# Performance work log

Hardware: AMD Instinct MI355X
Metric: run time of the kernel (lower is better)

The kernel has to match this reference:

```python
import jax, jax.numpy as jnp
jax.config.update("jax_enable_x64", True)
import numpy as np

BUCKETS = 2147483647  # max int32, as in fused_project call sites
HALF = BUCKETS >> 1
NGRAM_SIZE = 3
# sgnn partition boundaries: indices = [i*(i+1)/2 * P for i in range(n)] + [proj], P=112
IDX = [0, 112, 336, 672]


def _project(sig, mask, seeds):
    """One SgnnProjection partition.

    sig:   [B, M] int64 hash signatures in [0, BUCKETS) (padded ragged rows)
    mask:  [B, M] bool validity of each padded slot (ragged row structure)
    seeds: [H] int64 hash seeds
    returns [B, H] float32
    """
    # value = floormod(abs(sig * seed), buckets); center to [-half, half]
    v = jnp.abs(sig[None, :, :] * seeds[:, None, None]) % BUCKETS  # [H, B, M]
    v = v - jnp.where(v > HALF, BUCKETS, 0)
    vf = v.astype(jnp.float32) * mask[None].astype(jnp.float32)
    counts = jnp.maximum(mask.sum(-1), 1).astype(jnp.float32)  # [B], ragged row lengths
    mean = vf.sum(-1) / counts[None]  # [H, B]  (ragged reduce_mean)
    return (mean / HALF).T  # [B, H]


def setup_inputs() -> dict:
    key = jax.random.key(0)
    k1, k2, k3 = jax.random.split(key, 3)
    signatures = jax.random.randint(k1, (NGRAM_SIZE, 1024, 128), 0, BUCKETS, dtype=jnp.int64)
    mask = jax.random.bernoulli(k2, 0.7, (NGRAM_SIZE, 1024, 128))
    hash_seed = jax.random.randint(k3, (IDX[-1],), 1, BUCKETS, dtype=jnp.int64)
    return {"signatures": signatures, "mask": mask, "hash_seed": hash_seed}


def reference(signatures, mask, hash_seed):
    outs = [
        _project(signatures[i], mask[i], hash_seed[IDX[i]:IDX[i + 1]])
        for i in range(NGRAM_SIZE)
    ]
    return jnp.concatenate(outs, axis=-1).astype(jnp.float32)  # [B, 672]
```

## Files before the change

kernel.cpp:

```cpp
#include <hip/hip_runtime.h>


#define M31    2147483647u
#define HALF_B 1073741823u

__global__ __launch_bounds__(64) void sgnn_prep_kernel(
    const int* __restrict__ sig,
    const int* __restrict__ mask,
    unsigned* __restrict__ msig,
    float* __restrict__ invc,
    unsigned* __restrict__ cnt4)
{
    const int row = blockIdx.x;
    const int t   = threadIdx.x;
    const int g0  = row * 128 + t;
    const int g1  = g0 + 64;
    const int mk0 = mask[g0], mk1 = mask[g1];
    const unsigned v0 = (unsigned)sig[g0], v1 = (unsigned)sig[g1];

    const unsigned long long b0 = __ballot(mk0 != 0);
    const unsigned long long b1 = __ballot(mk1 != 0);
    const unsigned long long lt = (1ULL << t) - 1ULL;
    const int c0   = __popcll(b0);
    const int cnt  = c0 + __popcll(b1);
    const int pos0 = __popcll(b0 & lt);
    const int pos1 = c0 + __popcll(b1 & lt);

    const unsigned base = (unsigned)row * 128u;
    if (mk0) msig[base + pos0] = v0;
    if (mk1) msig[base + pos1] = v1;

    const int c4 = (cnt + 3) & ~3;
    if (cnt + t < c4) msig[base + cnt + t] = 0u;

    if (t == 0) {
        int c = (cnt < 1) ? 1 : cnt;
        invc[row] = 1.0f / ((float)c * 1073741823.0f);
        cnt4[row] = (unsigned)c4;
    }
}

__device__ __forceinline__ void acc_elem(unsigned sv ,
                                         unsigned seed ,
                                         unsigned long long& sum, unsigned& q) {
    const unsigned long long p2 =
        (unsigned long long)sv * (unsigned long long)seed + (unsigned long long)HALF_B;
    const unsigned lo = (unsigned)p2;
    const unsigned hi = (unsigned)(p2 >> 32);
    const unsigned s  = __builtin_amdgcn_alignbit(hi, lo, 31) + (lo & 0x7FFFFFFFu);
    q   += (s >= M31);
    sum += s;
}

__global__ __launch_bounds__(256, 4) void sgnn_main_kernel(
    const unsigned* __restrict__ msig,
    const float* __restrict__ invc,
    const unsigned* __restrict__ cnt4,
    const int* __restrict__ seeds,
    float* __restrict__ out,
    int nbatch)
{
    const unsigned tid  = threadIdx.x;
    const unsigned lane = tid & 63u;
    const unsigned W    = blockIdx.x * 4u + (tid >> 6);
    const unsigned b    = blockIdx.y;

    unsigned p, h0, hmax;
    if (W < 2u)      { p = 0; h0 = W * 64u;              hmax = 112u; }
    else if (W < 6u) { p = 1; h0 = 112u + (W - 2u) * 64u; hmax = 336u; }
    else             { p = 2; h0 = 336u + (W - 6u) * 64u; hmax = 672u; }

    const unsigned h     = h0 + lane;
    const bool     valid = (h < hmax);
    const unsigned h_c   = valid ? h : (hmax - 1u);

    const unsigned row_u = __builtin_amdgcn_readfirstlane(p * (unsigned)nbatch + b);
    const unsigned* __restrict__ rp = msig + (size_t)row_u * 128u;
    const unsigned n = cnt4[row_u];
    const unsigned seed = (unsigned)seeds[h_c];

    unsigned long long sum0 = 0, sum1 = 0;
    unsigned q0 = 0, q1 = 0;

    unsigned mm = 0;
    const unsigned n16 = n & ~15u;
    for (; mm < n16; mm += 16) {
        #pragma unroll
        for (unsigned jj = 0; jj < 16; jj += 2) {
            acc_elem(rp[mm + jj],     seed, sum0, q0);
            acc_elem(rp[mm + jj + 1], seed, sum1, q1);
        }
    }
    for (; mm < n; mm += 4) {
        #pragma unroll
        for (unsigned jj = 0; jj < 4; jj += 2) {
            acc_elem(rp[mm + jj],     seed, sum0, q0);
            acc_elem(rp[mm + jj + 1], seed, sum1, q1);
        }
    }

    if (valid) {
        const long long centered = (long long)(sum0 + sum1)
                                 - (long long)(q0 + q1) * 2147483647LL
                                 - (long long)n * 1073741823LL;
        out[b * 672u + h] = (float)centered * invc[row_u];
    }
}

extern "C" void kernel_launch(void* const* d_in, const int* in_sizes, int n_in,
                              void* d_out, int out_size, void* d_ws, size_t ws_size,
                              hipStream_t stream) {
    const int* sig   = (const int*)d_in[0];
    const int* mask  = (const int*)d_in[1];
    const int* seeds = (const int*)d_in[2];
    float* out = (float*)d_out;

    const int nbatch = in_sizes[0] / (3 * 128);
    const int nrows  = 3 * nbatch;
    unsigned* msig = (unsigned*)d_ws;
    float*    invc = (float*)((char*)d_ws + (size_t)nrows * 128 * 4);
    unsigned* c4   = (unsigned*)((char*)d_ws + (size_t)nrows * 132 * 4);

    sgnn_prep_kernel<<<dim3(nrows), dim3(64), 0, stream>>>(sig, mask, msig, invc, c4);
    sgnn_main_kernel<<<dim3(3, nbatch), dim3(256), 0, stream>>>(msig, invc, c4, seeds, out, nbatch);
}
```

Before: 77.33 us.

## Fuse mask compaction into main kernel via shared memory, simplify modular reduction

After: 73.70 us. -4.7%, faster.

```diff
diff --git a/kernel.cpp b/kernel.cpp
--- a/kernel.cpp
+++ b/kernel.cpp
@@ -4,69 +4,53 @@
 #define M31    2147483647u
 #define HALF_B 1073741823u
 
-__global__ __launch_bounds__(64) void sgnn_prep_kernel(
+__global__ __launch_bounds__(768) void sgnn_fused_kernel(
     const int* __restrict__ sig,
     const int* __restrict__ mask,
-    unsigned* __restrict__ msig,
-    float* __restrict__ invc,
-    unsigned* __restrict__ cnt4)
-{
-    const int row = blockIdx.x;
-    const int t   = threadIdx.x;
-    const int g0  = row * 128 + t;
-    const int g1  = g0 + 64;
-    const int mk0 = mask[g0], mk1 = mask[g1];
-    const unsigned v0 = (unsigned)sig[g0], v1 = (unsigned)sig[g1];
-
-    const unsigned long long b0 = __ballot(mk0 != 0);
-    const unsigned long long b1 = __ballot(mk1 != 0);
-    const unsigned long long lt = (1ULL << t) - 1ULL;
-    const int c0   = __popcll(b0);
-    const int cnt  = c0 + __popcll(b1);
-    const int pos0 = __popcll(b0 & lt);
-    const int pos1 = c0 + __popcll(b1 & lt);
-
-    const unsigned base = (unsigned)row * 128u;
-    if (mk0) msig[base + pos0] = v0;
-    if (mk1) msig[base + pos1] = v1;
-
-    const int c4 = (cnt + 3) & ~3;
-    if (cnt + t < c4) msig[base + cnt + t] = 0u;
-
-    if (t == 0) {
-        int c = (cnt < 1) ? 1 : cnt;
-        invc[row] = 1.0f / ((float)c * 1073741823.0f);
-        cnt4[row] = (unsigned)c4;
-    }
-}
-
-__device__ __forceinline__ void acc_elem(unsigned sv ,
-                                         unsigned seed ,
-                                         unsigned long long& sum, unsigned& q) {
-    const unsigned long long p2 =
-        (unsigned long long)sv * (unsigned long long)seed + (unsigned long long)HALF_B;
-    const unsigned lo = (unsigned)p2;
-    const unsigned hi = (unsigned)(p2 >> 32);
-    const unsigned s  = __builtin_amdgcn_alignbit(hi, lo, 31) + (lo & 0x7FFFFFFFu);
-    q   += (s >= M31);
-    sum += s;
-}
-
-__global__ __launch_bounds__(256, 4) void sgnn_main_kernel(
-    const unsigned* __restrict__ msig,
-    const float* __restrict__ invc,
-    const unsigned* __restrict__ cnt4,
     const int* __restrict__ seeds,
     float* __restrict__ out,
     int nbatch)
 {
+    __shared__ unsigned srow[3][128];
+    __shared__ float    sinv[3];
+    __shared__ unsigned sn[3];
+
     const unsigned tid  = threadIdx.x;
     const unsigned lane = tid & 63u;
-    const unsigned W    = blockIdx.x * 4u + (tid >> 6);
-    const unsigned b    = blockIdx.y;
+    const unsigned W    = tid >> 6;
+    const unsigned b    = blockIdx.x;
+
+    if (W < 3u) {
+        const unsigned rowg = W * (unsigned)nbatch + b;
+        const unsigned g0 = rowg * 128u + lane;
+        const unsigned g1 = g0 + 64u;
+        const int mk0 = mask[g0], mk1 = mask[g1];
+        const unsigned v0 = (unsigned)sig[g0], v1 = (unsigned)sig[g1];
+
+        const unsigned long long b0 = __ballot(mk0 != 0);
+        const unsigned long long b1 = __ballot(mk1 != 0);
+        const unsigned long long lt = (1ULL << lane) - 1ULL;
+        const int c0   = __popcll(b0);
+        const int cnt  = c0 + __popcll(b1);
+        const int pos0 = __popcll(b0 & lt);
+        const int pos1 = c0 + __popcll(b1 & lt);
+
+        if (mk0) srow[W][pos0] = v0;
+        if (mk1) srow[W][pos1] = v1;
+
+        const int c4 = (cnt + 3) & ~3;
+        if ((int)(cnt + lane) < c4) srow[W][cnt + lane] = 0u;
+
+        if (lane == 0) {
+            int c = (cnt < 1) ? 1 : cnt;
+            sinv[W] = 1.0f / ((float)c * 1073741823.0f);
+            sn[W]   = (unsigned)c4;
+        }
+    }
+    __syncthreads();
 
     unsigned p, h0, hmax;
-    if (W < 2u)      { p = 0; h0 = W * 64u;              hmax = 112u; }
+    if (W < 2u)      { p = 0; h0 = W * 64u;               hmax = 112u; }
     else if (W < 6u) { p = 1; h0 = 112u + (W - 2u) * 64u; hmax = 336u; }
     else             { p = 2; h0 = 336u + (W - 6u) * 64u; hmax = 672u; }
 
@@ -74,36 +58,96 @@
     const bool     valid = (h < hmax);
     const unsigned h_c   = valid ? h : (hmax - 1u);
 
-    const unsigned row_u = __builtin_amdgcn_readfirstlane(p * (unsigned)nbatch + b);
-    const unsigned* __restrict__ rp = msig + (size_t)row_u * 128u;
-    const unsigned n = cnt4[row_u];
-    const unsigned seed = (unsigned)seeds[h_c];
+    const unsigned long long seed = (unsigned long long)(unsigned)seeds[h_c];
+    const unsigned n = sn[p];
 
     unsigned long long sum0 = 0, sum1 = 0;
-    unsigned q0 = 0, q1 = 0;
-
     unsigned mm = 0;
-    const unsigned n16 = n & ~15u;
-    for (; mm < n16; mm += 16) {
-        #pragma unroll
-        for (unsigned jj = 0; jj < 16; jj += 2) {
-            acc_elem(rp[mm + jj],     seed, sum0, q0);
-            acc_elem(rp[mm + jj + 1], seed, sum1, q1);
+    const unsigned n8 = n & ~7u;
+    for (; mm < n8; mm += 8) {
+        const uint4 a = *(const uint4*)&srow[p][mm];
+        const uint4 c = *(const uint4*)&srow[p][mm + 4];
+        {
+            const unsigned long long p2 = (unsigned long long)a.x * seed + HALF_B;
+            const unsigned s = __builtin_amdgcn_alignbit((unsigned)(p2 >> 32), (unsigned)p2, 31)
+                             + ((unsigned)p2 & 0x7FFFFFFFu);
+            sum0 += min(s, s - M31);
+        }
+        {
+            const unsigned long long p2 = (unsigned long long)a.y * seed + HALF_B;
+            const unsigned s = __builtin_amdgcn_alignbit((unsigned)(p2 >> 32), (unsigned)p2, 31)
+                             + ((unsigned)p2 & 0x7FFFFFFFu);
+            sum1 += min(s, s - M31);
+        }
+        {
+            const unsigned long long p2 = (unsigned long long)a.z * seed + HALF_B;
+            const unsigned s = __builtin_amdgcn_alignbit((unsigned)(p2 >> 32), (unsigned)p2, 31)
+                             + ((unsigned)p2 & 0x7FFFFFFFu);
+            sum0 += min(s, s - M31);
+        }
+        {
+            const unsigned long long p2 = (unsigned long long)a.w * seed + HALF_B;
+            const unsigned s = __builtin_amdgcn_alignbit((unsigned)(p2 >> 32), (unsigned)p2, 31)
+                             + ((unsigned)p2 & 0x7FFFFFFFu);
+            sum1 += min(s, s - M31);
+        }
+        {
+            const unsigned long long p2 = (unsigned long long)c.x * seed + HALF_B;
+            const unsigned s = __builtin_amdgcn_alignbit((unsigned)(p2 >> 32), (unsigned)p2, 31)
+                             + ((unsigned)p2 & 0x7FFFFFFFu);
+            sum0 += min(s, s - M31);
+        }
+        {
+            const unsigned long long p2 = (unsigned long long)c.y * seed + HALF_B;
+            const unsigned s = __builtin_amdgcn_alignbit((unsigned)(p2 >> 32), (unsigned)p2, 31)
+                             + ((unsigned)p2 & 0x7FFFFFFFu);
+            sum1 += min(s, s - M31);
+        }
+        {
+            const unsigned long long p2 = (unsigned long long)c.z * seed + HALF_B;
+            const unsigned s = __builtin_amdgcn_alignbit((unsigned)(p2 >> 32), (unsigned)p2, 31)
+                             + ((unsigned)p2 & 0x7FFFFFFFu);
+            sum0 += min(s, s - M31);
+        }
+        {
+            const unsigned long long p2 = (unsigned long long)c.w * seed + HALF_B;
+            const unsigned s = __builtin_amdgcn_alignbit((unsigned)(p2 >> 32), (unsigned)p2, 31)
+                             + ((unsigned)p2 & 0x7FFFFFFFu);
+            sum1 += min(s, s - M31);
         }
     }
-    for (; mm < n; mm += 4) {
-        #pragma unroll
-        for (unsigned jj = 0; jj < 4; jj += 2) {
-            acc_elem(rp[mm + jj],     seed, sum0, q0);
-            acc_elem(rp[mm + jj + 1], seed, sum1, q1);
+    if (mm < n) {
+        const uint4 a = *(const uint4*)&srow[p][mm];
+        {
+            const unsigned long long p2 = (unsigned long long)a.x * seed + HALF_B;
+            const unsigned s = __builtin_amdgcn_alignbit((unsigned)(p2 >> 32), (unsigned)p2, 31)
+                             + ((unsigned)p2 & 0x7FFFFFFFu);
+            sum0 += min(s, s - M31);
+        }
+        {
+            const unsigned long long p2 = (unsigned long long)a.y * seed + HALF_B;
+            const unsigned s = __builtin_amdgcn_alignbit((unsigned)(p2 >> 32), (unsigned)p2, 31)
+                             + ((unsigned)p2 & 0x7FFFFFFFu);
+            sum1 += min(s, s - M31);
+        }
+        {
+            const unsigned long long p2 = (unsigned long long)a.z * seed + HALF_B;
+            const unsigned s = __builtin_amdgcn_alignbit((unsigned)(p2 >> 32), (unsigned)p2, 31)
+                             + ((unsigned)p2 & 0x7FFFFFFFu);
+            sum0 += min(s, s - M31);
+        }
+        {
+            const unsigned long long p2 = (unsigned long long)a.w * seed + HALF_B;
+            const unsigned s = __builtin_amdgcn_alignbit((unsigned)(p2 >> 32), (unsigned)p2, 31)
+                             + ((unsigned)p2 & 0x7FFFFFFFu);
+            sum1 += min(s, s - M31);
         }
     }
 
     if (valid) {
         const long long centered = (long long)(sum0 + sum1)
-                                 - (long long)(q0 + q1) * 2147483647LL
                                  - (long long)n * 1073741823LL;
-        out[b * 672u + h] = (float)centered * invc[row_u];
+        out[b * 672u + h] = (float)centered * sinv[p];
     }
 }
 
@@ -116,11 +160,5 @@
     float* out = (float*)d_out;
 
     const int nbatch = in_sizes[0] / (3 * 128);
-    const int nrows  = 3 * nbatch;
-    unsigned* msig = (unsigned*)d_ws;
-    float*    invc = (float*)((char*)d_ws + (size_t)nrows * 128 * 4);
-    unsigned* c4   = (unsigned*)((char*)d_ws + (size_t)nrows * 132 * 4);
-
-    sgnn_prep_kernel<<<dim3(nrows), dim3(64), 0, stream>>>(sig, mask, msig, invc, c4);
-    sgnn_main_kernel<<<dim3(3, nbatch), dim3(256), 0, stream>>>(msig, invc, c4, seeds, out, nbatch);
+    sgnn_fused_kernel<<<dim3(nbatch), dim3(768), 0, stream>>>(sig, mask, seeds, out, nbatch);
 }
```
